# Performance work log

Measured on AMD Instinct MI355X. Metric: run time of the kernel, lower is better.

The kernel has to match this reference:

```python
import jax, jax.numpy as jnp
import numpy as np

N_EMBED = 1024
HEAD_SIZE = 128
B, T = 8, 2048


def setup_inputs() -> dict:
    key = jax.random.key(0)
    kx, kk, kq, kv = jax.random.split(key, 4)
    x = jax.random.normal(kx, (B, T, N_EMBED), dtype=jnp.float32)
    Wk = jax.random.normal(kk, (N_EMBED, HEAD_SIZE), dtype=jnp.float32) * (N_EMBED ** -0.5)
    Wq = jax.random.normal(kq, (N_EMBED, HEAD_SIZE), dtype=jnp.float32) * (N_EMBED ** -0.5)
    Wv = jax.random.normal(kv, (N_EMBED, HEAD_SIZE), dtype=jnp.float32) * (N_EMBED ** -0.5)
    return {"x": x, "Wk": Wk, "Wq": Wq, "Wv": Wv}


def reference(x, Wk, Wq, Wv):
    # x: [B, T, C]; single-head causal attention, dropout rate 0 (identity)
    t = x.shape[1]
    k = jnp.einsum("btc,ch->bth", x, Wk)  # keys
    q = jnp.einsum("btc,ch->bth", x, Wq)  # queries
    v = jnp.einsum("btc,ch->bth", x, Wv)  # values
    scale = k.shape[-1] ** -0.5
    scores = jnp.einsum("bqh,bkh->bqk", q, k) * scale  # [B, T, T]
    causal = jnp.tril(jnp.ones((t, t), dtype=bool))
    scores = jnp.where(causal, scores, -jnp.inf)
    attn = jax.nn.softmax(scores, axis=-1)
    return jnp.einsum("bqk,bkh->bqh", attn, v)
```

## Files before the change

### kernel.cpp

```cpp
#include <hip/hip_runtime.h>
#include <hip/hip_bf16.h>
#include <math.h>

#define B_ 8
#define T_ 2048
#define C_ 1024
#define D_ 128
#define M_ (B_*T_)

typedef __attribute__((ext_vector_type(8))) short short8;
typedef __attribute__((ext_vector_type(4))) short sshort4;
typedef __attribute__((ext_vector_type(4))) float floatx4;
typedef __hip_bfloat16 bf16;

#define QSCALE 0.12751744416218247f

__global__ __launch_bounds__(256) void cvt_w2_kernel(const float* __restrict__ Wq,
                                                     const float* __restrict__ Wk,
                                                     const float* __restrict__ Wv,
                                                     bf16* __restrict__ Wt) {
    __shared__ bf16 tl[64][136];
    const int t = threadIdx.x;
    const int k0 = blockIdx.x * 64, g = blockIdx.y;
    const float* W = (g == 0) ? Wq : (g == 1) ? Wk : Wv;
    {
        int k = t >> 2, n0 = (t & 3) * 32;
        const float* src = W + (size_t)(k0 + k) * 128 + n0;
#pragma unroll
        for (int j = 0; j < 4; ++j) {
            float4 v0 = *(const float4*)(src + j * 8);
            float4 v1 = *(const float4*)(src + j * 8 + 4);
            union { short8 s; __hip_bfloat162 h[4]; } u;
            __hip_bfloat162 h;
            h.x = __float2bfloat16(v0.x); h.y = __float2bfloat16(v0.y); u.h[0] = h;
            h.x = __float2bfloat16(v0.z); h.y = __float2bfloat16(v0.w); u.h[1] = h;
            h.x = __float2bfloat16(v1.x); h.y = __float2bfloat16(v1.y); u.h[2] = h;
            h.x = __float2bfloat16(v1.z); h.y = __float2bfloat16(v1.w); u.h[3] = h;
            *(short8*)&tl[k][n0 + j * 8] = u.s;
        }
    }
    __syncthreads();
    {
        int n = t >> 1, ko = (t & 1) * 32;
        union { short8 s[4]; bf16 e[32]; } u;
#pragma unroll
        for (int i = 0; i < 32; ++i) u.e[i] = tl[ko + i][n];
        bf16* dst = Wt + (size_t)g * 131072 + (size_t)n * 1024 + k0 + ko;
#pragma unroll
        for (int j = 0; j < 4; ++j) *(short8*)(dst + j * 8) = u.s[j];
    }
}

__global__ __launch_bounds__(512, 4) void proj6_kernel(const float* __restrict__ x,
                                                       const bf16* __restrict__ Wt,
                                                       bf16* __restrict__ Qb,
                                                       bf16* __restrict__ Kb,
                                                       bf16* __restrict__ Vt) {
    __shared__ bf16 la[32][72];
    __shared__ bf16 lb[384][72];
    const int t = threadIdx.x;
    const int wave = t >> 6, lane = t & 63;
    const int quad = lane >> 4, l15 = lane & 15;
    const int wr2 = wave >> 2, wc2 = wave & 3;
    const int row0 = blockIdx.x * 32;
    const int ar = t >> 4, ao = (t & 15) * 4;

    floatx4 acc[6];
#pragma unroll
    for (int n = 0; n < 6; ++n) acc[n] = (floatx4)0.0f;

    float4 xr;
    short8 wreg[6];
    {
        xr = *(const float4*)(x + (size_t)(row0 + ar) * 1024 + ao);
#pragma unroll
        for (int j = 0; j < 6; ++j) {
            int c = t + j * 512;
            int rb = c >> 3, ob = (c & 7) * 8;
            wreg[j] = *(const short8*)(Wt + (size_t)rb * 1024 + ob);
        }
    }

    for (int kc = 0; kc < 16; ++kc) {
        __syncthreads();
        {
            union { sshort4 s; __hip_bfloat162 h[2]; } u;
            __hip_bfloat162 h;
            h.x = __float2bfloat16(xr.x); h.y = __float2bfloat16(xr.y); u.h[0] = h;
            h.x = __float2bfloat16(xr.z); h.y = __float2bfloat16(xr.w); u.h[1] = h;
            *(sshort4*)&la[ar][ao] = u.s;
        }
#pragma unroll
        for (int j = 0; j < 6; ++j) {
            int c = t + j * 512;
            int rb = c >> 3, ob = (c & 7) * 8;
            *(short8*)&lb[rb][ob] = wreg[j];
        }
        if (kc < 15) {
            xr = *(const float4*)(x + (size_t)(row0 + ar) * 1024 + (kc + 1) * 64 + ao);
#pragma unroll
            for (int j = 0; j < 6; ++j) {
                int c = t + j * 512;
                int rb = c >> 3, ob = (c & 7) * 8;
                wreg[j] = *(const short8*)(Wt + (size_t)rb * 1024 + (kc + 1) * 64 + ob);
            }
        }
        __syncthreads();
#pragma unroll
        for (int dk = 0; dk < 2; ++dk) {
            short8 af, bff[6];
            af = *(const short8*)&la[wr2 * 16 + l15][dk * 32 + quad * 8];
#pragma unroll
            for (int n = 0; n < 6; ++n) bff[n] = *(const short8*)&lb[wc2 * 96 + n * 16 + l15][dk * 32 + quad * 8];
#pragma unroll
            for (int n = 0; n < 6; ++n)
                acc[n] = __builtin_amdgcn_mfma_f32_16x16x32_bf16(af, bff[n], acc[n], 0, 0, 0);
        }
    }

    __syncthreads();
    bf16* vtl = &lb[0][0];
#pragma unroll
    for (int r = 0; r < 4; ++r) {
        const int tt = wr2 * 16 + quad * 4 + r;
        const int row = row0 + tt;
#pragma unroll
        for (int n = 0; n < 6; ++n) {
            const int colb = wc2 * 96 + n * 16;
            const int g = colb >> 7;
            const int lc = (colb & 127) + l15;
            const float v = acc[n][r];
            if (g == 0)      Qb[(size_t)row * 128 + lc] = __float2bfloat16(v * QSCALE);
            else if (g == 1) Kb[(size_t)row * 128 + lc] = __float2bfloat16(v);
            else             vtl[tt * 136 + lc] = __float2bfloat16(v);
        }
    }
    __syncthreads();
    {
        int d = t & 127, toff = (t >> 7) * 8;
        union { short8 s; bf16 e[8]; } u;
#pragma unroll
        for (int i = 0; i < 8; ++i) u.e[i] = vtl[(toff + i) * 136 + d];
        int bb = row0 >> 11, t0 = row0 & 2047;
        *(short8*)(Vt + (size_t)(bb * D_ + d) * T_ + t0 + toff) = u.s;
    }
}

__global__ __launch_bounds__(256, 3) void flash_fm2_kernel(const bf16* __restrict__ Qb,
                                                           const bf16* __restrict__ Kb,
                                                           const bf16* __restrict__ Vt,
                                                           float* __restrict__ out,
                                                           bf16* __restrict__ Opart,
                                                           float* __restrict__ Lpart) {
    const int tile = blockIdx.x, seg = blockIdx.y, b = blockIdx.z;
    const int keys_total = (tile + 1) * 64;
    const int nseg = (keys_total + 255) >> 8;
    if (seg >= nseg) return;

    __shared__ bf16 lds_k[64][136];
    __shared__ bf16 lds_v[128][72];
    __shared__ bf16 lds_p[4][16][72];
    const int t = threadIdx.x;
    const int wave = t >> 6, lane = t & 63;
    const int quad = lane >> 4, l15 = lane & 15;
    const int q0 = tile * 64;
    const int k_start = seg << 8;
    const int k_end = min(k_start + 256, keys_total);
    const int nch = (k_end - k_start) >> 6;

    short8 qf[4];
    {
        int qm = q0 + wave * 16 + l15;
#pragma unroll
        for (int dk = 0; dk < 4; ++dk)
            qf[dk] = *(const short8*)(Qb + (size_t)(b * T_ + qm) * 128 + dk * 32 + quad * 8);
    }

    short8 kreg[4], vreg[4];
    {
        const int k0 = k_start;
#pragma unroll
        for (int j = 0; j < 4; ++j) {
            int c = t + j * 256;
            { int r = c >> 4, co = (c & 15) * 8;
              kreg[j] = *(const short8*)(Kb + (size_t)(b * T_ + k0 + r) * 128 + co); }
            { int d = c >> 3, co = (c & 7) * 8;
              vreg[j] = *(const short8*)(Vt + (size_t)b * (D_ * T_) + d * T_ + k0 + co); }
        }
    }

    floatx4 o_acc[8];
#pragma unroll
    for (int i = 0; i < 8; ++i) o_acc[i] = (floatx4)0.0f;
    float lp[4] = {0.f, 0.f, 0.f, 0.f};
    const int qrow = q0 + wave * 16 + quad * 4;

    for (int ch = 0; ch < nch; ++ch) {
        const int k0 = k_start + (ch << 6);
        __syncthreads();
#pragma unroll
        for (int j = 0; j < 4; ++j) {
            int c = t + j * 256;
            { int r = c >> 4, co = (c & 15) * 8; *(short8*)&lds_k[r][co] = kreg[j]; }
            { int d = c >> 3, co = (c & 7) * 8;  *(short8*)&lds_v[d][co] = vreg[j]; }
        }
        if (ch + 1 < nch) {
            const int kn = k0 + 64;
#pragma unroll
            for (int j = 0; j < 4; ++j) {
                int c = t + j * 256;
                { int r = c >> 4, co = (c & 15) * 8;
                  kreg[j] = *(const short8*)(Kb + (size_t)(b * T_ + kn + r) * 128 + co); }
                { int d = c >> 3, co = (c & 7) * 8;
                  vreg[j] = *(const short8*)(Vt + (size_t)b * (D_ * T_) + d * T_ + kn + co); }
            }
        }
        __syncthreads();

        floatx4 s[4];
#pragma unroll
        for (int nt = 0; nt < 4; ++nt) s[nt] = (floatx4)0.0f;
#pragma unroll
        for (int dk = 0; dk < 4; ++dk)
#pragma unroll
            for (int nt = 0; nt < 4; ++nt) {
                short8 kb = *(const short8*)&lds_k[nt * 16 + l15][dk * 32 + quad * 8];
                s[nt] = __builtin_amdgcn_mfma_f32_16x16x32_bf16(qf[dk], kb, s[nt], 0, 0, 0);
            }

        float sv[4][4];
#pragma unroll
        for (int nt = 0; nt < 4; ++nt)
#pragma unroll
            for (int r = 0; r < 4; ++r) sv[nt][r] = s[nt][r];

        if (k0 + 63 > q0) {
#pragma unroll
            for (int nt = 0; nt < 4; ++nt) {
                int key = k0 + nt * 16 + l15;
#pragma unroll
                for (int r = 0; r < 4; ++r)
                    if (key > qrow + r) sv[nt][r] = -1e30f;
            }
        }

#pragma unroll
        for (int nt = 0; nt < 4; ++nt)
#pragma unroll
            for (int r = 0; r < 4; ++r) sv[nt][r] = exp2f(sv[nt][r]);
#pragma unroll
        for (int r = 0; r < 4; ++r)
            lp[r] += (sv[0][r] + sv[1][r]) + (sv[2][r] + sv[3][r]);

#pragma unroll
        for (int nt = 0; nt < 4; ++nt)
#pragma unroll
            for (int r = 0; r < 4; ++r)
                lds_p[wave][quad * 4 + r][nt * 16 + l15] = __float2bfloat16(sv[nt][r]);
        short8 pa0 = *(const short8*)&lds_p[wave][l15][quad * 8];
        short8 pa1 = *(const short8*)&lds_p[wave][l15][32 + quad * 8];

#pragma unroll
        for (int nt = 0; nt < 8; ++nt) {
            short8 vb0 = *(const short8*)&lds_v[nt * 16 + l15][quad * 8];
            short8 vb1 = *(const short8*)&lds_v[nt * 16 + l15][32 + quad * 8];
            o_acc[nt] = __builtin_amdgcn_mfma_f32_16x16x32_bf16(pa0, vb0, o_acc[nt], 0, 0, 0);
            o_acc[nt] = __builtin_amdgcn_mfma_f32_16x16x32_bf16(pa1, vb1, o_acc[nt], 0, 0, 0);
        }
    }

    float l_i[4];
#pragma unroll
    for (int r = 0; r < 4; ++r) {
        float v = lp[r];
        v += __shfl_xor(v, 1);
        v += __shfl_xor(v, 2);
        v += __shfl_xor(v, 4);
        v += __shfl_xor(v, 8);
        l_i[r] = v;
    }

    const int lrow = wave * 16 + quad * 4;
    if (nseg == 1) {
        float inv_l[4];
#pragma unroll
        for (int r = 0; r < 4; ++r) inv_l[r] = 1.0f / l_i[r];
#pragma unroll
        for (int f = 0; f < 8; ++f)
#pragma unroll
            for (int r = 0; r < 4; ++r)
                out[(size_t)(b * T_ + qrow + r) * 128 + f * 16 + l15] = o_acc[f][r] * inv_l[r];
    } else {
        int pre = 0;
        for (int u = 4; u < tile; ++u) pre += (u + 4) >> 2;
        const size_t slot = (size_t)b * 140 + pre + seg;
        bf16* ob = Opart + slot * (64 * 128);
#pragma unroll
        for (int f = 0; f < 8; ++f)
#pragma unroll
            for (int r = 0; r < 4; ++r)
                ob[(size_t)(lrow + r) * 128 + f * 16 + l15] = __float2bfloat16(o_acc[f][r]);
        if (l15 == 0) {
#pragma unroll
            for (int r = 0; r < 4; ++r)
                Lpart[slot * 64 + lrow + r] = l_i[r];
        }
    }
}

__global__ __launch_bounds__(256) void combine4_kernel(const bf16* __restrict__ Opart,
                                                       const float* __restrict__ Lpart,
                                                       float* __restrict__ out) {
    const int tile = blockIdx.x + 4, b = blockIdx.y;
    const int nseg = (tile + 4) >> 2;
    int pre = 0;
    for (int u = 4; u < tile; ++u) pre += (u + 4) >> 2;
    const size_t slot0 = (size_t)b * 140 + pre;
    const int t = threadIdx.x;
    const int row = t >> 2, c0 = (t & 3) * 32;

    float lsum = 0.f;
    for (int j = 0; j < nseg; ++j) lsum += Lpart[(slot0 + j) * 64 + row];

    float acc[32];
#pragma unroll
    for (int i = 0; i < 32; ++i) acc[i] = 0.f;
    for (int j = 0; j < nseg; ++j) {
        const bf16* src = Opart + (slot0 + j) * (64 * 128) + (size_t)row * 128 + c0;
#pragma unroll
        for (int u = 0; u < 4; ++u) {
            short8 v8 = *(const short8*)(src + u * 8);
#pragma unroll
            for (int e = 0; e < 8; ++e) {
                union { unsigned int u32; float f; } cv;
                cv.u32 = ((unsigned int)(unsigned short)v8[e]) << 16;
                acc[u * 8 + e] += cv.f;
            }
        }
    }
    float inv = 1.0f / lsum;
    float* dst = out + (size_t)(b * T_ + tile * 64 + row) * 128 + c0;
#pragma unroll
    for (int i = 0; i < 32; ++i) dst[i] = acc[i] * inv;
}

extern "C" void kernel_launch(void* const* d_in, const int* in_sizes, int n_in,
                              void* d_out, int out_size, void* d_ws, size_t ws_size,
                              hipStream_t stream) {
    const float* x  = (const float*)d_in[0];
    const float* Wk = (const float*)d_in[1];
    const float* Wq = (const float*)d_in[2];
    const float* Wv = (const float*)d_in[3];
    float* out = (float*)d_out;

    char* ws = (char*)d_ws;
    bf16*  Wt    = (bf16*)ws;
    bf16*  Qb    = (bf16*)(ws + 786432);
    bf16*  Kb    = (bf16*)(ws + 4980736);
    bf16*  Vt    = (bf16*)(ws + 9175040);
    bf16*  Opart = (bf16*)(ws + 13369344);
    float* Lpart = (float*)(ws + 31719424);

    cvt_w2_kernel<<<dim3(16, 3), 256, 0, stream>>>(Wq, Wk, Wv, Wt);
    proj6_kernel<<<512, 512, 0, stream>>>(x, Wt, Qb, Kb, Vt);
    flash_fm2_kernel<<<dim3(32, 8, B_), 256, 0, stream>>>(Qb, Kb, Vt, out, Opart, Lpart);
    combine4_kernel<<<dim3(28, B_), 256, 0, stream>>>(Opart, Lpart, out);
}
```

Baseline: 87.40 us.

## Retile QKV projection to 128x96 block tiles with 4x3 MFMA per wave

Result: slower. 105.5 us (+20.7%).

```diff
diff --git a/kernel.cpp b/kernel.cpp
--- a/kernel.cpp
+++ b/kernel.cpp
@@ -51,98 +51,132 @@
     }
 }
 
-__global__ __launch_bounds__(512, 4) void proj6_kernel(const float* __restrict__ x,
+__global__ __launch_bounds__(256, 2) void proj7_kernel(const float* __restrict__ x,
                                                        const bf16* __restrict__ Wt,
                                                        bf16* __restrict__ Qb,
                                                        bf16* __restrict__ Kb,
                                                        bf16* __restrict__ Vt) {
-    __shared__ bf16 la[32][72];
-    __shared__ bf16 lb[384][72];
+    __shared__ bf16 smem[16128];
+    bf16* la = smem;
+    bf16* lb = smem + 9216;
     const int t = threadIdx.x;
     const int wave = t >> 6, lane = t & 63;
     const int quad = lane >> 4, l15 = lane & 15;
-    const int wr2 = wave >> 2, wc2 = wave & 3;
-    const int row0 = blockIdx.x * 32;
-    const int ar = t >> 4, ao = (t & 15) * 4;
-
-    floatx4 acc[6];
-#pragma unroll
-    for (int n = 0; n < 6; ++n) acc[n] = (floatx4)0.0f;
-
-    float4 xr;
-    short8 wreg[6];
+    const int wr = wave >> 1, wc = wave & 1;
+    const int rt = blockIdx.x >> 2, cg = blockIdx.x & 3;
+    const int row0 = rt * 128, col0 = cg * 96;
+    const int xrow = t & 127, xko = (t >> 7) * 32;
+
+    floatx4 acc[4][3];
+#pragma unroll
+    for (int m = 0; m < 4; ++m)
+#pragma unroll
+        for (int n = 0; n < 3; ++n) acc[m][n] = (floatx4)0.0f;
+
+    float4 xf[8];
+    short8 wreg[3];
     {
-        xr = *(const float4*)(x + (size_t)(row0 + ar) * 1024 + ao);
-#pragma unroll
-        for (int j = 0; j < 6; ++j) {
-            int c = t + j * 512;
+        const float* src = x + (size_t)(row0 + xrow) * 1024 + xko;
+#pragma unroll
+        for (int j = 0; j < 8; ++j) xf[j] = *(const float4*)(src + j * 4);
+#pragma unroll
+        for (int j = 0; j < 3; ++j) {
+            int c = t + j * 256;
             int rb = c >> 3, ob = (c & 7) * 8;
-            wreg[j] = *(const short8*)(Wt + (size_t)rb * 1024 + ob);
+            wreg[j] = *(const short8*)(Wt + (size_t)(col0 + rb) * 1024 + ob);
         }
     }
 
     for (int kc = 0; kc < 16; ++kc) {
         __syncthreads();
-        {
-            union { sshort4 s; __hip_bfloat162 h[2]; } u;
+#pragma unroll
+        for (int j = 0; j < 4; ++j) {
+            union { short8 s; __hip_bfloat162 h[4]; } u;
             __hip_bfloat162 h;
-            h.x = __float2bfloat16(xr.x); h.y = __float2bfloat16(xr.y); u.h[0] = h;
-            h.x = __float2bfloat16(xr.z); h.y = __float2bfloat16(xr.w); u.h[1] = h;
-            *(sshort4*)&la[ar][ao] = u.s;
-        }
-#pragma unroll
-        for (int j = 0; j < 6; ++j) {
-            int c = t + j * 512;
+            h.x = __float2bfloat16(xf[2 * j].x);     h.y = __float2bfloat16(xf[2 * j].y);     u.h[0] = h;
+            h.x = __float2bfloat16(xf[2 * j].z);     h.y = __float2bfloat16(xf[2 * j].w);     u.h[1] = h;
+            h.x = __float2bfloat16(xf[2 * j + 1].x); h.y = __float2bfloat16(xf[2 * j + 1].y); u.h[2] = h;
+            h.x = __float2bfloat16(xf[2 * j + 1].z); h.y = __float2bfloat16(xf[2 * j + 1].w); u.h[3] = h;
+            *(short8*)&la[xrow * 72 + xko + j * 8] = u.s;
+        }
+#pragma unroll
+        for (int j = 0; j < 3; ++j) {
+            int c = t + j * 256;
             int rb = c >> 3, ob = (c & 7) * 8;
-            *(short8*)&lb[rb][ob] = wreg[j];
+            *(short8*)&lb[rb * 72 + ob] = wreg[j];
         }
         if (kc < 15) {
-            xr = *(const float4*)(x + (size_t)(row0 + ar) * 1024 + (kc + 1) * 64 + ao);
+            const float* src = x + (size_t)(row0 + xrow) * 1024 + (kc + 1) * 64 + xko;
+#pragma unroll
+            for (int j = 0; j < 8; ++j) xf[j] = *(const float4*)(src + j * 4);
+#pragma unroll
+            for (int j = 0; j < 3; ++j) {
+                int c = t + j * 256;
+                int rb = c >> 3, ob = (c & 7) * 8;
+                wreg[j] = *(const short8*)(Wt + (size_t)(col0 + rb) * 1024 + (kc + 1) * 64 + ob);
+            }
+        }
+        __syncthreads();
+#pragma unroll
+        for (int dk = 0; dk < 2; ++dk) {
+            short8 af[4], bff[3];
+#pragma unroll
+            for (int m = 0; m < 4; ++m) af[m] = *(const short8*)&la[(wr * 64 + m * 16 + l15) * 72 + dk * 32 + quad * 8];
+#pragma unroll
+            for (int n = 0; n < 3; ++n) bff[n] = *(const short8*)&lb[(wc * 48 + n * 16 + l15) * 72 + dk * 32 + quad * 8];
+#pragma unroll
+            for (int m = 0; m < 4; ++m)
+#pragma unroll
+                for (int n = 0; n < 3; ++n)
+                    acc[m][n] = __builtin_amdgcn_mfma_f32_16x16x32_bf16(af[m], bff[n], acc[m][n], 0, 0, 0);
+        }
+    }
+
+    __syncthreads();
+    bf16* vtl = smem;
+    const int vstride = (cg == 2) ? 40 : 104;
+    const int vdbase  = (cg == 2) ? 0 : 32;
+#pragma unroll
+    for (int m = 0; m < 4; ++m)
+#pragma unroll
+        for (int r = 0; r < 4; ++r) {
+            const int tt = wr * 64 + m * 16 + quad * 4 + r;
+            const int row = row0 + tt;
+#pragma unroll
+            for (int n = 0; n < 3; ++n) {
+                const int colg = col0 + wc * 48 + n * 16;
+                const int g = colg >> 7;
+                const int lc = (colg & 127) + l15;
+                const float v = acc[m][n][r];
+                if (g == 0)      Qb[(size_t)row * 128 + lc] = __float2bfloat16(v * QSCALE);
+                else if (g == 1) Kb[(size_t)row * 128 + lc] = __float2bfloat16(v);
+                else             vtl[tt * vstride + (lc - vdbase)] = __float2bfloat16(v);
+            }
+        }
+    if (cg >= 2) {
+        __syncthreads();
+        const int bb = row0 >> 11, t0 = row0 & 2047;
+        if (cg == 2) {
+#pragma unroll
+            for (int j = 0; j < 2; ++j) {
+                int c = t + j * 256;
+                int d = c & 31, rowblk = c >> 5;
+                union { short8 s; bf16 e[8]; } u;
+#pragma unroll
+                for (int i = 0; i < 8; ++i) u.e[i] = vtl[(rowblk * 8 + i) * 40 + d];
+                *(short8*)(Vt + ((size_t)bb * D_ + d) * T_ + t0 + rowblk * 8) = u.s;
+            }
+        } else {
 #pragma unroll
             for (int j = 0; j < 6; ++j) {
-                int c = t + j * 512;
-                int rb = c >> 3, ob = (c & 7) * 8;
-                wreg[j] = *(const short8*)(Wt + (size_t)rb * 1024 + (kc + 1) * 64 + ob);
-            }
-        }
-        __syncthreads();
-#pragma unroll
-        for (int dk = 0; dk < 2; ++dk) {
-            short8 af, bff[6];
-            af = *(const short8*)&la[wr2 * 16 + l15][dk * 32 + quad * 8];
-#pragma unroll
-            for (int n = 0; n < 6; ++n) bff[n] = *(const short8*)&lb[wc2 * 96 + n * 16 + l15][dk * 32 + quad * 8];
-#pragma unroll
-            for (int n = 0; n < 6; ++n)
-                acc[n] = __builtin_amdgcn_mfma_f32_16x16x32_bf16(af, bff[n], acc[n], 0, 0, 0);
-        }
-    }
-
-    __syncthreads();
-    bf16* vtl = &lb[0][0];
-#pragma unroll
-    for (int r = 0; r < 4; ++r) {
-        const int tt = wr2 * 16 + quad * 4 + r;
-        const int row = row0 + tt;
-#pragma unroll
-        for (int n = 0; n < 6; ++n) {
-            const int colb = wc2 * 96 + n * 16;
-            const int g = colb >> 7;
-            const int lc = (colb & 127) + l15;
-            const float v = acc[n][r];
-            if (g == 0)      Qb[(size_t)row * 128 + lc] = __float2bfloat16(v * QSCALE);
-            else if (g == 1) Kb[(size_t)row * 128 + lc] = __float2bfloat16(v);
-            else             vtl[tt * 136 + lc] = __float2bfloat16(v);
-        }
-    }
-    __syncthreads();
-    {
-        int d = t & 127, toff = (t >> 7) * 8;
-        union { short8 s; bf16 e[8]; } u;
-#pragma unroll
-        for (int i = 0; i < 8; ++i) u.e[i] = vtl[(toff + i) * 136 + d];
-        int bb = row0 >> 11, t0 = row0 & 2047;
-        *(short8*)(Vt + (size_t)(bb * D_ + d) * T_ + t0 + toff) = u.s;
+                int c = t + j * 256;
+                int d = c % 96, rowblk = c / 96;
+                union { short8 s; bf16 e[8]; } u;
+#pragma unroll
+                for (int i = 0; i < 8; ++i) u.e[i] = vtl[(rowblk * 8 + i) * 104 + d];
+                *(short8*)(Vt + ((size_t)bb * D_ + 32 + d) * T_ + t0 + rowblk * 8) = u.s;
+            }
+        }
     }
 }
 
@@ -362,7 +396,7 @@
     float* Lpart = (float*)(ws + 31719424);
 
     cvt_w2_kernel<<<dim3(16, 3), 256, 0, stream>>>(Wq, Wk, Wv, Wt);
-    proj6_kernel<<<512, 512, 0, stream>>>(x, Wt, Qb, Kb, Vt);
+    proj7_kernel<<<512, 256, 0, stream>>>(x, Wt, Qb, Kb, Vt);
     flash_fm2_kernel<<<dim3(32, 8, B_), 256, 0, stream>>>(Qb, Kb, Vt, out, Opart, Lpart);
     combine4_kernel<<<dim3(28, B_), 256, 0, stream>>>(Opart, Lpart, out);
 }
```
